# Kernel optimization log

Hardware: AMD Instinct MI355X
Metric: run time of the kernel (lower is better)

Reference implementation:

```python
import jax, jax.numpy as jnp
import numpy as np

THRE = 0.5        # communication threshold
ALPHA = 0.8       # S_e / S_c mix in pattern gate
P_BIAS, P_WEIGHT = 0.1, 0.9
DILATE_K = 3
EPS = 1e-6


def warp_affine(src, M, out_hw):
    """torch F.affine_grid + F.grid_sample (bilinear, zeros padding, align_corners=False).
    src: (B,C,Hs,Ws), M: (B,2,3) normalized affine. Returns (B,C,Ho,Wo)."""
    B, C, Hs, Ws = src.shape
    Ho, Wo = out_hw
    xs = 2.0 * (jnp.arange(Wo, dtype=src.dtype) + 0.5) / Wo - 1.0
    ys = 2.0 * (jnp.arange(Ho, dtype=src.dtype) + 0.5) / Ho - 1.0
    gx, gy = jnp.meshgrid(xs, ys)                                   # (Ho,Wo)
    base = jnp.stack([gx, gy, jnp.ones_like(gx)], axis=-1)          # (Ho,Wo,3)
    g = jnp.einsum('bij,hwj->bhwi', M.astype(src.dtype), base)      # (B,Ho,Wo,2) x,y
    px = ((g[..., 0] + 1.0) * Ws - 1.0) * 0.5
    py = ((g[..., 1] + 1.0) * Hs - 1.0) * 0.5
    x0 = jnp.floor(px); y0 = jnp.floor(py)
    wx1 = px - x0; wx0 = 1.0 - wx1
    wy1 = py - y0; wy0 = 1.0 - wy1
    bidx = jnp.arange(B)[:, None, None]
    def samp(yi, xi):
        yi = yi.astype(jnp.int32); xi = xi.astype(jnp.int32)
        valid = (yi >= 0) & (yi < Hs) & (xi >= 0) & (xi < Ws)
        yc = jnp.clip(yi, 0, Hs - 1); xc = jnp.clip(xi, 0, Ws - 1)
        v = src[bidx, :, yc, xc]                                    # (B,Ho,Wo,C)
        return v * valid[..., None].astype(src.dtype)
    out = (samp(y0, x0) * (wy0 * wx0)[..., None]
         + samp(y0, x0 + 1) * (wy0 * wx1)[..., None]
         + samp(y0 + 1, x0) * (wy1 * wx0)[..., None]
         + samp(y0 + 1, x0 + 1) * (wy1 * wx1)[..., None])
    return jnp.transpose(out, (0, 3, 1, 2))


def masked_quantile(xf, mf, q):
    """torch.quantile(x[mask], q) with linear interpolation. xf:(N,HW) float, mf:(N,HW) bool."""
    xs = jnp.sort(jnp.where(mf, xf, jnp.inf), axis=-1)
    cnt = mf.sum(axis=-1)
    pos = q * jnp.maximum(cnt - 1, 0).astype(xf.dtype)
    lo = jnp.floor(pos).astype(jnp.int32)
    hi = jnp.ceil(pos).astype(jnp.int32)
    frac = pos - lo.astype(xf.dtype)
    vlo = jnp.take_along_axis(xs, lo[:, None], axis=-1)[:, 0]
    vhi = jnp.take_along_axis(xs, hi[:, None], axis=-1)[:, 0]
    val = vlo + frac * (vhi - vlo)
    return jnp.where(cnt > 0, val, jnp.zeros_like(val))


def qnorm01(x, mask, ql=0.2, qh=0.8):
    """_qnorm01_masked: per-image masked quantile normalization to [0,1]."""
    N = x.shape[0]
    xf = x.reshape(N, -1)
    mf = mask.reshape(N, -1) > 0
    lo = masked_quantile(xf, mf, ql)[:, None]
    hi = masked_quantile(xf, mf, qh)[:, None]
    y = jnp.clip((xf - lo) / (hi - lo + EPS), 0.0, 1.0) * mf.astype(x.dtype)
    return y.reshape(x.shape)


def pattern_gate(conf_b, feats_b, vis_b):
    """_build_pattern_gate. Returns P (1,1,H,W) on ego plane."""
    visf = (vis_b > 0).astype(feats_b.dtype)
    energy = jnp.mean(feats_b ** 2, axis=1, keepdims=True)          # (N,1,H,W)
    S_e = qnorm01(energy, vis_b) * visf
    S_c_raw = jnp.max(jax.nn.sigmoid(conf_b), axis=1, keepdims=True)  # A>1 branch
    S_c = qnorm01(S_c_raw, vis_b) * visf
    S_mix = ALPHA * S_e + (1.0 - ALPHA) * S_c
    D_e = qnorm01(1.0 - S_e[0:1], vis_b[0:1])
    D_c = qnorm01(1.0 - S_c[0:1], vis_b[0:1])
    D = (0.7 * D_e + 0.3 * D_c) * visf[0:1]
    m0 = vis_b[0:1].reshape(1, -1) > 0
    q20_e = masked_quantile(S_e[0:1].reshape(1, -1), m0, 0.2)[0]
    q20_c = masked_quantile(S_c[0:1].reshape(1, -1), m0, 0.2)[0]
    Ke = (S_e[0:1] <= q20_e) & (vis_b[0:1] > 0)
    Kc = (S_c[0:1] <= q20_c) & (vis_b[0:1] > 0)
    K_empty = (Ke & Kc).astype(feats_b.dtype)
    Sup_nei = jnp.mean(S_mix[1:] * visf[1:], axis=0, keepdims=True)
    P = D * Sup_nei * (1.0 - K_empty)
    return qnorm01(P, vis_b[0:1]) * visf[0:1]


def dilate(mask, k):
    if k <= 1:
        return mask
    return jax.lax.reduce_window(mask, -jnp.inf, jax.lax.max,
                                 (1, 1, k, k), (1, 1, 1, 1), 'SAME')


def owner_for_batch(feats_b, conf_b, vis_b, base_b):
    """_compute_owner_masks_from_comm for one batch group (N agents), eval mode
    (soft_tau=0 -> hard argmax owner), dual_ratio=0, dilate_k=3, supply='cls'."""
    N = feats_b.shape[0]
    visf = (vis_b > 0).astype(feats_b.dtype)
    S_full = jnp.clip(conf_b, 0.0, 1.0).mean(axis=1, keepdims=True) * visf
    P = pattern_gate(conf_b, feats_b, vis_b)                        # (1,1,H,W)
    S_b = S_full * (P_BIAS + P_WEIGHT * P)                          # broadcast over N
    scores = S_b * visf                                             # (N,1,H,W)
    winner = jnp.argmax(scores, axis=0)                             # (1,H,W)
    onehot = (jnp.arange(N)[:, None, None, None] == winner[None]).astype(feats_b.dtype)
    owner = onehot * (base_b > 0).astype(feats_b.dtype)
    return dilate(owner, DILATE_K)


def forward(x, psm_single, record_len, normalized_affine_matrix):
    B, L = normalized_affine_matrix.shape[:2]
    N = L  # uniform record_len assumed (record_len[b] == L for all b)
    sumN, C, H, W = x.shape
    A = psm_single.shape[1]
    # ego-view warp matrices t_matrix[0, :N] per batch, flattened to (B*N,2,3)
    M = normalized_affine_matrix[:, 0].reshape(B * N, 2, 3)
    ones = jnp.ones((B * N, 1, H, W), x.dtype)
    vis = warp_affine(ones, M, (H, W))          # warp masks
    conf = warp_affine(psm_single, M, (H, W))   # warped confidence maps
    wx = warp_affine(x, M, (H, W))              # warped features
    # Communication: where2comm-style threshold on max-sigmoid confidence; ego always ones
    comm_map = jnp.max(jax.nn.sigmoid(conf), axis=1, keepdims=True)
    comm = (comm_map > THRE).astype(x.dtype)
    comm = comm.reshape(B, N, 1, H, W).at[:, 0].set(1.0)            # (B,N,1,H,W)
    owner = jax.vmap(owner_for_batch)(
        wx.reshape(B, N, C, H, W), conf.reshape(B, N, A, H, W),
        vis.reshape(B, N, 1, H, W), comm)                           # (B,N,1,H,W)
    final = comm * owner
    wxm = wx.reshape(B, N, C, H, W) * final
    # effective rate over non-ego agents
    eff = final[:, 1:].sum(axis=(1, 2, 3, 4)) / ((N - 1) * H * W)
    effective_rate = eff.mean()
    x_out = wxm.max(axis=1)                                         # MaxFusion over agents
    return x_out, effective_rate


def setup_inputs():
    key = jax.random.key(0)
    k1, k2, k3 = jax.random.split(key, 3)
    B, N, C, A, H, W = 4, 5, 64, 2, 128, 256
    x = jax.random.normal(k1, (B * N, C, H, W), jnp.float32)
    psm_single = jax.random.normal(k2, (B * N, A, H, W), jnp.float32)
    record_len = jnp.full((B,), N, jnp.int32)
    eye = jnp.tile(jnp.array([[1.0, 0.0, 0.0], [0.0, 1.0, 0.0]], jnp.float32), (B, N, N, 1, 1))
    mats = eye + 0.05 * jax.random.normal(k3, (B, N, N, 2, 3), jnp.float32)
    return {"x": x, "psm_single": psm_single, "record_len": record_len,
            "normalized_affine_matrix": mats}


def reference(x, psm_single, record_len, normalized_affine_matrix):
    return forward(x, psm_single, record_len, normalized_affine_matrix)
```

## Files before the change

### kernel.cpp

```cpp
#include <hip/hip_runtime.h>

#define W_    256
#define H_    128
#define HW_   32768
#define NB    4
#define NA    5
#define NC    64
#define NIMG  20
#define EPS_  1e-6f

#define TW    32
#define TH    16
#define CAP   2048
#define TRIPS 2
#define NBUF  3

struct Taps { int o00,o01,o10,o11; float w00,w01,w10,w11; };

__device__ inline void proj_pt(float M0,float M1,float M2,float M3,float M4,float M5,
                               int h,int w,float&px,float&py){
  float gx = 2.0f*((float)w+0.5f)/(float)W_ - 1.0f;
  float gy = 2.0f*((float)h+0.5f)/(float)H_ - 1.0f;
  float X = M0*gx + M1*gy + M2;
  float Y = M3*gx + M4*gy + M5;
  px = ((X+1.0f)*(float)W_ - 1.0f)*0.5f;
  py = ((Y+1.0f)*(float)H_ - 1.0f)*0.5f;
}

__device__ inline Taps make_taps(const float* __restrict__ M, int h, int w){
  float px,py; proj_pt(M[0],M[1],M[2],M[3],M[4],M[5],h,w,px,py);
  float x0f=floorf(px), y0f=floorf(py);
  float wx1=px-x0f, wx0=1.f-wx1, wy1=py-y0f, wy0=1.f-wy1;
  int x0=(int)x0f, y0=(int)y0f, x1=x0+1, y1=y0+1;
  bool vx0=(x0>=0)&&(x0<W_), vx1=(x1>=0)&&(x1<W_);
  bool vy0=(y0>=0)&&(y0<H_), vy1=(y1>=0)&&(y1<H_);
  int cx0=min(max(x0,0),W_-1), cx1=min(max(x1,0),W_-1);
  int cy0=min(max(y0,0),H_-1), cy1=min(max(y1,0),H_-1);
  Taps t;
  t.o00=cy0*W_+cx0; t.o01=cy0*W_+cx1; t.o10=cy1*W_+cx0; t.o11=cy1*W_+cx1;
  t.w00=(vy0&&vx0)?(wy0*wx0):0.f;
  t.w01=(vy0&&vx1)?(wy0*wx1):0.f;
  t.w10=(vy1&&vx0)?(wy1*wx0):0.f;
  t.w11=(vy1&&vx1)?(wy1*wx1):0.f;
  return t;
}

__device__ inline float clip01(float v){ return fminf(fmaxf(v,0.f),1.f); }
__device__ inline float sigmoidf_(float v){
  if (v>=0.f){ float e=expf(-v); return 1.f/(1.f+e); }
  float e=expf(v); return e/(1.f+e);
}
__device__ inline float quantv(int cnt, float q, float vlo, float vhi){
  if (cnt<=0) return 0.f;
  float pos = q*(float)(cnt-1);
  float frac = pos - floorf(pos);
  return vlo + frac*(vhi-vlo);
}
__device__ inline float ge_f(float t, float lo, float hi){
  return clip01((t-lo)/(hi-lo+EPS_));
}

#define SBAR __builtin_amdgcn_sched_barrier(0)

__global__ void k_init(int* counters){ if (threadIdx.x < 1+NIMG) counters[threadIdx.x] = 0; }

__global__ __launch_bounds__(256) void k_warp_stats(
  const float* __restrict__ x, const float* __restrict__ psm, const float* __restrict__ nam,
  float* __restrict__ vis, float* __restrict__ scraw, float* __restrict__ sfull,
  float* __restrict__ energy, int* __restrict__ cntv)
{
  __shared__ __align__(16) float smem[NBUF][CAP];
  int tid = threadIdx.x;
  int tx = blockIdx.x, ty = blockIdx.y, bn = blockIdx.z;
  int b = bn/NA, n = bn - b*NA;
  const float* M = nam + (size_t)(b*NA*NA + n)*6;
  float M0=M[0],M1=M[1],M2=M[2],M3=M[3],M4=M[4],M5=M[5];
  int tw0 = tx*TW, th0 = ty*TH;
  int r  = tid>>4;
  int cb = (tid&15)<<1;
  int h  = th0 + r;
  int w0 = tw0 + cb;

  float pxa,pya,pxb,pyb,pxc,pyc,pxd,pyd;
  proj_pt(M0,M1,M2,M3,M4,M5, th0,      tw0,      pxa,pya);
  proj_pt(M0,M1,M2,M3,M4,M5, th0,      tw0+TW-1, pxb,pyb);
  proj_pt(M0,M1,M2,M3,M4,M5, th0+TH-1, tw0,      pxc,pyc);
  proj_pt(M0,M1,M2,M3,M4,M5, th0+TH-1, tw0+TW-1, pxd,pyd);
  float pxmin=fminf(fminf(pxa,pxb),fminf(pxc,pxd));
  float pxmax=fmaxf(fmaxf(pxa,pxb),fmaxf(pxc,pxd));
  float pymin=fminf(fminf(pya,pyb),fminf(pyc,pyd));
  float pymax=fmaxf(fmaxf(pya,pyb),fmaxf(pyc,pyd));
  int xs = min(max((int)floorf(pxmin)-1, 0), W_-1);
  int xe = min(max((int)floorf(pxmax)+2, 0), W_-1);
  int ys = min(max((int)floorf(pymin)-1, 0), H_-1);
  int ye = min(max((int)floorf(pymax)+2, 0), H_-1);
  int xs4 = xs & ~3;
  int bwid = xe - xs4 + 1, bh = ye - ys + 1;
  int nck = (bwid+3)>>2;
  int bwp = nck<<2;
  int E2 = bh*bwp;
  bool ok = (E2 <= CAP);

  float vvv[2], w00_[2],w01_[2],w10_[2],w11_[2];
  int   gx0[2],gx1[2],gy0c[2],gy1c[2];
  int   rx0[2]; bool vx0f[2];
  #pragma unroll
  for (int k=0;k<2;++k){
    float px,py; proj_pt(M0,M1,M2,M3,M4,M5, h, w0+k, px,py);
    float x0f=floorf(px), y0f=floorf(py);
    float wx1=px-x0f, wx0=1.f-wx1, wy1=py-y0f, wy0=1.f-wy1;
    int x0=(int)x0f, y0=(int)y0f, x1=x0+1, y1=y0+1;
    bool vx0=(x0>=0)&&(x0<W_), vx1=(x1>=0)&&(x1<W_);
    bool vy0=(y0>=0)&&(y0<H_), vy1=(y1>=0)&&(y1<H_);
    float w00=(vy0&&vx0)?(wy0*wx0):0.f;
    float w01=(vy0&&vx1)?(wy0*wx1):0.f;
    float w10=(vy1&&vx0)?(wy1*wx0):0.f;
    float w11=(vy1&&vx1)?(wy1*wx1):0.f;
    w00_[k]=w00; w01_[k]=w01; w10_[k]=w10; w11_[k]=w11;
    vvv[k]=w00+w01+w10+w11;
    gx0[k]=min(max(x0,0),W_-1); gx1[k]=min(max(x1,0),W_-1);
    gy0c[k]=min(max(y0,0),H_-1); gy1c[k]=min(max(y1,0),H_-1);
    rx0[k]=x0; vx0f[k]=vx0;
  }

  size_t idx = (size_t)bn*HW_ + (size_t)h*W_ + w0;
  float acc[2] = {0.f,0.f};

  int srcoff[TRIPS]; int ldsbase = (tid>>6)<<6;
  const float* xb0 = x + (size_t)bn*NC*HW_ + (size_t)ys*W_ + xs4;
  if (ok){
    int totq = bh*nck;
    unsigned magic = (unsigned)((0x100000000ULL + (unsigned)nck - 1) / (unsigned)nck);
    int colcap = (W_-4) - xs4;
    #pragma unroll
    for (int k=0;k<TRIPS;++k){
      int qq = min(tid + (k<<8), totq-1);
      int row = (int)__umulhi((unsigned)qq, magic);
      int col = (qq - row*nck)<<2;
      srcoff[k] = row*W_ + min(col, colcap);
    }
  }
  auto issue = [&](int ch, int bsel){
    const float* src = xb0 + (size_t)ch*HW_;
    #pragma unroll
    for (int k=0;k<TRIPS;++k){
      __builtin_amdgcn_global_load_lds(
        (const __attribute__((address_space(1))) void*)(src + srcoff[k]),
        (__attribute__((address_space(3))) void*)&smem[bsel][(ldsbase + (k<<8))<<2],
        16, 0, 0);
    }
  };
  if (ok){ issue(0,0); issue(1,1); }

  {
    const float* p0 = psm + ((size_t)bn*2+0)*HW_;
    const float* p1 = psm + ((size_t)bn*2+1)*HW_;
    int vsum = 0;
    #pragma unroll
    for (int k=0;k<2;++k){
      int o00=gy0c[k]*W_+gx0[k], o01=gy0c[k]*W_+gx1[k];
      int o10=gy1c[k]*W_+gx0[k], o11=gy1c[k]*W_+gx1[k];
      float c0 = w00_[k]*p0[o00]+w01_[k]*p0[o01]+w10_[k]*p0[o10]+w11_[k]*p0[o11];
      float c1 = w00_[k]*p1[o00]+w01_[k]*p1[o01]+w10_[k]*p1[o10]+w11_[k]*p1[o11];
      vis[idx+k]   = vvv[k];
      scraw[idx+k] = fmaxf(sigmoidf_(c0), sigmoidf_(c1));
      sfull[idx+k] = (clip01(c0)+clip01(c1))*0.5f;
      vsum += (vvv[k]>0.f)?1:0;
    }
    #pragma unroll
    for (int off=32;off;off>>=1) vsum += __shfl_down(vsum,off);
    if ((tid&63)==0) atomicAdd(&cntv[bn], vsum);
  }

  if (ok){
    int a0[2],a1[2]; float e0[2],e1[2],f0[2],f1[2];
    #pragma unroll
    for (int k=0;k<2;++k){
      int bc = min(max(rx0[k]-xs4,0), bwp-1);
      a0[k] = (gy0c[k]-ys)*bwp + bc;
      a1[k] = (gy1c[k]-ys)*bwp + bc;
      bool v0 = vx0f[k];
      e0[k] = v0 ? w00_[k] : w01_[k];
      e1[k] = v0 ? w01_[k] : 0.f;
      f0[k] = v0 ? w10_[k] : w11_[k];
      f1[k] = v0 ? w11_[k] : 0.f;
    }
    #pragma unroll 1
    for (int c=0;c<NC;++c){
      asm volatile("s_waitcnt vmcnt(2)" ::: "memory"); SBAR;
      __builtin_amdgcn_s_barrier(); SBAR;
      {
        int nc2 = c+2 < NC ? c+2 : NC-1;
        issue(nc2, (c+2)%NBUF);
      }
      const float* B = smem[c%NBUF];
      #pragma unroll
      for (int k=0;k<2;++k){
        float r00=B[a0[k]], r01=B[a0[k]+1];
        float r10=B[a1[k]], r11=B[a1[k]+1];
        float v = e0[k]*r00 + e1[k]*r01 + f0[k]*r10 + f1[k]*r11;
        acc[k] += v*v;
      }
    }
    asm volatile("s_waitcnt vmcnt(0)" ::: "memory");
  } else {
    const float* xb = x + (size_t)bn*NC*HW_;
    int go00[2],go01[2],go10[2],go11[2];
    #pragma unroll
    for (int k=0;k<2;++k){
      go00[k]=gy0c[k]*W_+gx0[k]; go01[k]=gy0c[k]*W_+gx1[k];
      go10[k]=gy1c[k]*W_+gx0[k]; go11[k]=gy1c[k]*W_+gx1[k];
    }
    for (int c=0;c<NC;++c){
      const float* pc = xb + (size_t)c*HW_;
      #pragma unroll
      for (int k=0;k<2;++k){
        float v = w00_[k]*pc[go00[k]] + w01_[k]*pc[go01[k]]
                + w10_[k]*pc[go10[k]] + w11_[k]*pc[go11[k]];
        acc[k] += v*v;
      }
    }
  }
  #pragma unroll
  for (int k=0;k<2;++k) energy[idx+k] = acc[k]*(1.0f/64.0f);
}

#define OS_T 1024
__global__ __launch_bounds__(1024) void k_select(
    const float* __restrict__ energy, const float* __restrict__ scraw,
    const float* __restrict__ ppre, const float* __restrict__ vis,
    const int* __restrict__ cnts,
    float* __restrict__ statsE, float* __restrict__ statsC, float* __restrict__ statsP,
    int mode)
{
  __shared__ int hist[16*256];
  __shared__ int cum[256];
  __shared__ unsigned s_pre;
  __shared__ int s_rk;
  int tid = threadIdx.x;
  int t = blockIdx.x;

  const float* d; const float* m; float* stats; int img, r, cnt;
  if (mode==0){
    bool isC = (t>=96); int tt = isC ? t-96 : t;
    if (tt<80){ img=tt>>2; r=tt&3; } else { int j=tt-80; img=(j>>2)*NA; r=4+(j&3); }
    d = (isC?scraw:energy) + (size_t)img*HW_;
    m = vis + (size_t)img*HW_;
    stats = isC?statsC:statsE;
    cnt = cnts[img];
  } else {
    img = t>>2; r = t&3;
    d = ppre + (size_t)img*HW_;
    m = vis + (size_t)(img*NA)*HW_;
    stats = statsP;
    cnt = cnts[img*NA];
  }
  int cm1 = cnt>0 ? cnt-1 : 0;
  float p2 = 0.2f*(float)cm1, p8 = 0.8f*(float)cm1;
  int l2=(int)floorf(p2), h2=(int)ceilf(p2), l8=(int)floorf(p8), h8=(int)ceilf(p8);
  int rank;
  switch(r){
    case 0: rank=l2; break;      case 1: rank=h2; break;
    case 2: rank=l8; break;      case 3: rank=h8; break;
    case 4: rank=cm1-l2; break;  case 5: rank=cm1-h2; break;
    case 6: rank=cm1-l8; break;  default: rank=cm1-h8; break;
  }

  unsigned key[32];
  #pragma unroll
  for (int k=0;k<32;++k){
    int i = tid + (k<<10);
    unsigned u = __float_as_uint(d[i]);
    unsigned kk = (u & 0x80000000u) ? ~u : (u|0x80000000u);
    key[k] = (m[i] > 0.f) ? kk : 0xFFFFFFFFu;
  }

  if (tid==0){ s_pre=0u; s_rk=rank; }
  int slice = tid & 15;
  #pragma unroll
  for (int round=0; round<4; ++round){
    const int shift = 24 - 8*round;
    for (int i=tid;i<16*256;i+=OS_T) hist[i]=0;
    __syncthreads();
    unsigned pre = s_pre;
    if (round==0){
      #pragma unroll
      for (int k=0;k<32;++k)
        atomicAdd(&hist[slice*256 + (key[k]>>24)], 1);
    } else {
      #pragma unroll
      for (int k=0;k<32;++k)
        if ((key[k]>>(shift+8)) == pre)
          atomicAdd(&hist[slice*256 + ((key[k]>>shift)&255u)], 1);
    }
    __syncthreads();
    if (tid<256){
      int tt=0;
      #pragma unroll
      for (int s=0;s<16;++s) tt += hist[s*256+tid];
      cum[tid]=tt;
    }
    __syncthreads();
    if (tid<64){
      int c0=cum[4*tid+0],c1=cum[4*tid+1],c2=cum[4*tid+2],c3=cum[4*tid+3];
      int i0=c0, i1=i0+c1, i2=i1+c2, i3=i2+c3;
      int tot=i3, scan=tot;
      #pragma unroll
      for (int off=1;off<64;off<<=1){ int v=__shfl_up(scan,off); if (tid>=off) scan+=v; }
      int base = scan-tot;
      int rk = s_rk; unsigned pr = s_pre;
      int b0=base, b1=base+i0, b2=base+i1, b3=base+i2, e3=base+i3;
      if      (rk>=b0 && rk<b1){ s_pre=(pr<<8)|(unsigned)(4*tid+0); s_rk=rk-b0; }
      else if (rk>=b1 && rk<b2){ s_pre=(pr<<8)|(unsigned)(4*tid+1); s_rk=rk-b1; }
      else if (rk>=b2 && rk<b3){ s_pre=(pr<<8)|(unsigned)(4*tid+2); s_rk=rk-b2; }
      else if (rk>=b3 && rk<e3){ s_pre=(pr<<8)|(unsigned)(4*tid+3); s_rk=rk-b3; }
    }
    __syncthreads();
  }
  if (tid==0){
    unsigned k = s_pre;
    unsigned u = (k & 0x80000000u) ? (k & 0x7FFFFFFFu) : ~k;
    stats[img*16 + 1 + r] = __uint_as_float(u);
    if (r==0) stats[img*16] = (float)cnt;
  }
}

__global__ void k_params(const float* __restrict__ statsE, const float* __restrict__ statsC,
                         float* __restrict__ params){
  int b = threadIdx.x;
  if (b>=NB) return;
  float* pr = params + b*32;
  for (int n=0;n<NA;++n){
    const float* sE = statsE + (size_t)(b*NA+n)*16;
    const float* sC = statsC + (size_t)(b*NA+n)*16;
    int cE=(int)sE[0], cC=(int)sC[0];
    pr[n]    = quantv(cE,0.2f,sE[1],sE[2]);
    pr[5+n]  = quantv(cE,0.8f,sE[3],sE[4]);
    pr[10+n] = quantv(cC,0.2f,sC[1],sC[2]);
    pr[15+n] = quantv(cC,0.8f,sC[3],sC[4]);
  }
  const float* sE0 = statsE + (size_t)(b*NA)*16;
  const float* sC0 = statsC + (size_t)(b*NA)*16;
  float loe=pr[0], hie=pr[5], loc=pr[10], hic=pr[15];
  float de_lo=0.f,de_hi=0.f,ke=0.f, dc_lo=0.f,dc_hi=0.f,kc=0.f;
  int c0=(int)sE0[0];
  if (c0>0){
    int cm1=c0-1;
    float pos2=0.2f*(float)cm1, pos8=0.8f*(float)cm1;
    float f2=pos2-floorf(pos2), f8=pos8-floorf(pos8);
    float a,bb;
    a=1.f-ge_f(sE0[5],loe,hie); bb=1.f-ge_f(sE0[6],loe,hie); de_lo=a+f2*(bb-a);
    a=1.f-ge_f(sE0[7],loe,hie); bb=1.f-ge_f(sE0[8],loe,hie); de_hi=a+f8*(bb-a);
    a=ge_f(sE0[1],loe,hie);     bb=ge_f(sE0[2],loe,hie);     ke  =a+f2*(bb-a);
  }
  int c0c=(int)sC0[0];
  if (c0c>0){
    int cm1=c0c-1;
    float pos2=0.2f*(float)cm1, pos8=0.8f*(float)cm1;
    float f2=pos2-floorf(pos2), f8=pos8-floorf(pos8);
    float a,bb;
    a=1.f-ge_f(sC0[5],loc,hic); bb=1.f-ge_f(sC0[6],loc,hic); dc_lo=a+f2*(bb-a);
    a=1.f-ge_f(sC0[7],loc,hic); bb=1.f-ge_f(sC0[8],loc,hic); dc_hi=a+f8*(bb-a);
    a=ge_f(sC0[1],loc,hic);     bb=ge_f(sC0[2],loc,hic);     kc  =a+f2*(bb-a);
  }
  pr[20]=de_lo; pr[21]=de_hi; pr[22]=dc_lo; pr[23]=dc_hi; pr[24]=ke; pr[25]=kc;
}

__global__ __launch_bounds__(256) void k_ppre(
  const float* __restrict__ vis, const float* __restrict__ scraw,
  const float* __restrict__ energy, const float* __restrict__ params,
  float* __restrict__ ppre)
{
  int w=threadIdx.x, h=blockIdx.x, b=blockIdx.y;
  int p=h*W_+w;
  const float* pr = params + b*32;
  size_t base = (size_t)b*NA*HW_ + p;
  float se[NA], sc[NA], vf[NA];
  #pragma unroll
  for (int n=0;n<NA;++n){
    float vv = vis[base + (size_t)n*HW_];
    float f = (vv>0.f)?1.f:0.f; vf[n]=f;
    se[n] = clip01((energy[base+(size_t)n*HW_]-pr[n])/(pr[5+n]-pr[n]+EPS_))*f;
    sc[n] = clip01((scraw[base+(size_t)n*HW_]-pr[10+n])/(pr[15+n]-pr[10+n]+EPS_))*f;
  }
  float sup = 0.f;
  #pragma unroll
  for (int n=1;n<NA;++n) sup += (0.8f*se[n]+0.2f*sc[n])*vf[n];
  sup *= 0.25f;
  float de = clip01(((1.f-se[0])-pr[20])/(pr[21]-pr[20]+EPS_))*vf[0];
  float dc = clip01(((1.f-sc[0])-pr[22])/(pr[23]-pr[22]+EPS_))*vf[0];
  float D  = (0.7f*de + 0.3f*dc)*vf[0];
  bool ke = (se[0] <= pr[24]) && (vf[0]>0.f);
  bool kc = (sc[0] <= pr[25]) && (vf[0]>0.f);
  float kem = (ke&&kc)?1.f:0.f;
  ppre[(size_t)b*HW_+p] = D*sup*(1.f-kem);
}

__global__ __launch_bounds__(256) void k_owner(
  const float* __restrict__ vis, const float* __restrict__ scraw,
  const float* __restrict__ sfull, const float* __restrict__ ppre,
  const float* __restrict__ statsP, int* __restrict__ omask)
{
  int w=threadIdx.x,h=blockIdx.x,b=blockIdx.y;
  int p=h*W_+w;
  const float* sP = statsP + b*16;
  int cntP=(int)sP[0];
  float plo = quantv(cntP,0.2f,sP[1],sP[2]);
  float phi = quantv(cntP,0.8f,sP[3],sP[4]);
  size_t base=(size_t)b*NA*HW_+p;
  float vf0 = (vis[base]>0.f)?1.f:0.f;
  float Pf = clip01((ppre[(size_t)b*HW_+p]-plo)/(phi-plo+EPS_))*vf0;
  float gate = 0.1f + 0.9f*Pf;
  int winner=0; float best=-1.f;
  int cbits=0;
  #pragma unroll
  for (int n=0;n<NA;++n){
    float vv = vis[base+(size_t)n*HW_];
    float f=(vv>0.f)?1.f:0.f;
    float s = ((sfull[base+(size_t)n*HW_]*f)*gate)*f;
    if (s>best){best=s;winner=n;}
    bool cm = (n==0) || (scraw[base+(size_t)n*HW_] > 0.5f);
    if (cm) cbits |= 1<<n;
  }
  int ob = ((cbits>>winner)&1) ? (1<<winner) : 0;
  omask[(size_t)b*HW_+p] = ob | (cbits<<8);
}

__global__ __launch_bounds__(256) void k_final(
  const int* __restrict__ omask, int* __restrict__ fmask, int* __restrict__ counter)
{
  int w=threadIdx.x,h=blockIdx.x,b=blockIdx.y;
  int p=h*W_+w;
  const int* om = omask + (size_t)b*HW_;
  int ow=0;
  #pragma unroll
  for (int dy=-1;dy<=1;++dy){
    int y=h+dy; if (y<0||y>=H_) continue;
    #pragma unroll
    for (int dx=-1;dx<=1;++dx){
      int x=w+dx; if (x<0||x>=W_) continue;
      ow |= om[y*W_+x];
    }
  }
  int cbits=(om[p]>>8)&31;
  int fin = ow & cbits & 31;
  fmask[(size_t)b*HW_+p]=fin;
  int cn = __popc(fin & 30);
  for (int off=32;off;off>>=1) cn += __shfl_down(cn,off);
  if ((threadIdx.x&63)==0) atomicAdd(counter, cn);
}

__global__ __launch_bounds__(256, 2) void k_out(
  const float* __restrict__ x, const float* __restrict__ nam,
  const int* __restrict__ fmask, const int* __restrict__ counter,
  float* __restrict__ out, int out_size)
{
  int w=threadIdx.x, h=blockIdx.x, b=blockIdx.y;
  int p=h*W_+w;
  int fin = fmask[(size_t)b*HW_+p] & 31;
  float init = (__popc(fin)<NA) ? 0.f : -__builtin_inff();
  Taps tp[NA];
  #pragma unroll
  for (int n=0;n<NA;++n) tp[n] = make_taps(nam + (size_t)(b*NA*NA+n)*6, h, w);
  #pragma unroll 1
  for (int cb=0; cb<NC/16; ++cb){
    float m[16];
    #pragma unroll
    for (int c=0;c<16;++c) m[c]=init;
    #pragma unroll
    for (int n=0;n<NA;++n){
      if (!((fin>>n)&1)) continue;
      const float* pc = x + ((size_t)(b*NA+n)*NC + cb*16)*HW_;
      float a00[16],a01[16],a10[16],a11[16];
      #pragma unroll
      for (int c=0;c<16;++c){
        a00[c]=pc[tp[n].o00]; a01[c]=pc[tp[n].o01]; a10[c]=pc[tp[n].o10]; a11[c]=pc[tp[n].o11];
        pc += HW_;
      }
      #pragma unroll
      for (int c=0;c<16;++c){
        float v = tp[n].w00*a00[c] + tp[n].w01*a01[c] + tp[n].w10*a10[c] + tp[n].w11*a11[c];
        m[c] = fmaxf(m[c], v);
      }
    }
    #pragma unroll
    for (int c=0;c<16;++c)
      out[(((size_t)b*NC + cb*16 + c)*H_+h)*W_+w] = m[c];
  }
  if (b==0 && h==0 && w==0)
    out[out_size-1] = (float)(*counter) * (1.0f/524288.0f);
}

extern "C" void kernel_launch(void* const* d_in, const int* in_sizes, int n_in,
                              void* d_out, int out_size, void* d_ws, size_t ws_size,
                              hipStream_t stream) {
  (void)in_sizes; (void)n_in; (void)ws_size;
  const float* x   = (const float*)d_in[0];
  const float* psm = (const float*)d_in[1];
  const float* nam = (const float*)d_in[3];
  float* out = (float*)d_out;

  float* ws     = (float*)d_ws;
  float* vis    = ws;
  float* scraw  = vis    + (size_t)NIMG*HW_;
  float* sfull  = scraw  + (size_t)NIMG*HW_;
  float* energy = sfull  + (size_t)NIMG*HW_;
  float* ppre   = energy + (size_t)NIMG*HW_;
  float* statsE = ppre   + (size_t)NB*HW_;
  float* statsC = statsE + NIMG*16;
  float* statsP = statsC + NIMG*16;
  float* params = statsP + NB*16;
  int*   omask  = (int*)(params + NB*32);
  int*   fmask  = omask + (size_t)NB*HW_;
  int*   counter= fmask + (size_t)NB*HW_;
  int*   cntv   = counter + 1;

  hipLaunchKernelGGL(k_init, dim3(1), dim3(64), 0, stream, counter);
  hipLaunchKernelGGL(k_warp_stats, dim3(W_/TW, H_/TH, NIMG), dim3(256), 0, stream,
                     x, psm, nam, vis, scraw, sfull, energy, cntv);
  hipLaunchKernelGGL(k_select, dim3(192), dim3(OS_T), 0, stream,
                     energy, scraw, ppre, vis, cntv, statsE, statsC, statsP, 0);
  hipLaunchKernelGGL(k_params, dim3(1), dim3(64), 0, stream, statsE, statsC, params);
  hipLaunchKernelGGL(k_ppre, dim3(H_,NB), dim3(W_), 0, stream,
                     vis, scraw, energy, params, ppre);
  hipLaunchKernelGGL(k_select, dim3(16), dim3(OS_T), 0, stream,
                     energy, scraw, ppre, vis, cntv, statsE, statsC, statsP, 1);
  hipLaunchKernelGGL(k_owner, dim3(H_,NB), dim3(W_), 0, stream,
                     vis, scraw, sfull, ppre, statsP, omask);
  hipLaunchKernelGGL(k_final, dim3(H_,NB), dim3(W_), 0, stream, omask, fmask, counter);
  hipLaunchKernelGGL(k_out, dim3(H_,NB), dim3(W_), 0, stream,
                     x, nam, fmask, counter, out, out_size);
}
```

Measured before the change: 249.6 us.

## Compute warped energy from precomputed local Gram products instead of per-channel sampling

Energy is the channel-mean of the squared bilinear warp. The change expands that square into a quadratic form over the four taps. A new kernel precomputes per-pixel channel sums of squares and of neighbour cross-products (right, down, both diagonals) in a single coalesced pass over x. A second per-pixel kernel then combines these with the bilinear weights, which removes the per-channel LDS-staged gather loop. The cost is five extra full-size workspace buffers and an extra launch, and the fast path only runs when the workspace is large enough; otherwise it falls back to the old kernel.

```diff
diff --git a/kernel.cpp b/kernel.cpp
--- a/kernel.cpp
+++ b/kernel.cpp
@@ -8,12 +8,6 @@
 #define NC    64
 #define NIMG  20
 #define EPS_  1e-6f
-
-#define TW    32
-#define TH    16
-#define CAP   2048
-#define TRIPS 2
-#define NBUF  3
 
 struct Taps { int o00,o01,o10,o11; float w00,w01,w10,w11; };
 
@@ -64,28 +58,124 @@
 
 __global__ void k_init(int* counters){ if (threadIdx.x < 1+NIMG) counters[threadIdx.x] = 0; }
 
-__global__ __launch_bounds__(256) void k_warp_stats(
+__global__ __launch_bounds__(128) void k_gram(
+  const float* __restrict__ x, float* __restrict__ gA, float* __restrict__ gBx,
+  float* __restrict__ gBy, float* __restrict__ gBd1, float* __restrict__ gBd2)
+{
+  int tid = threadIdx.x;
+  int lane = tid & 63;
+  int bx = blockIdx.x;
+  int bn = bx >> 6;
+  int slab = bx & 63;
+  int r  = slab*2 + (tid>>6);
+  int rn = min(r+1, H_-1);
+  int col = lane<<2;
+  const float* xb = x + (size_t)bn*NC*HW_;
+  float4 aA={0,0,0,0}, aBx={0,0,0,0}, aBy={0,0,0,0}, aBd1={0,0,0,0}, aBd2={0,0,0,0};
+  #pragma unroll 4
+  for (int c=0;c<NC;++c){
+    const float* pc = xb + (size_t)c*HW_;
+    float4 a = *reinterpret_cast<const float4*>(pc + r*W_  + col);
+    float4 b = *reinterpret_cast<const float4*>(pc + rn*W_ + col);
+    float axn = __shfl(a.x, lane+1, 64);
+    float bxn = __shfl(b.x, lane+1, 64);
+    aA.x  = fmaf(a.x,a.x,aA.x);  aA.y  = fmaf(a.y,a.y,aA.y);
+    aA.z  = fmaf(a.z,a.z,aA.z);  aA.w  = fmaf(a.w,a.w,aA.w);
+    aBx.x = fmaf(a.x,a.y,aBx.x); aBx.y = fmaf(a.y,a.z,aBx.y);
+    aBx.z = fmaf(a.z,a.w,aBx.z); aBx.w = fmaf(a.w,axn,aBx.w);
+    aBy.x = fmaf(a.x,b.x,aBy.x); aBy.y = fmaf(a.y,b.y,aBy.y);
+    aBy.z = fmaf(a.z,b.z,aBy.z); aBy.w = fmaf(a.w,b.w,aBy.w);
+    aBd1.x= fmaf(a.x,b.y,aBd1.x);aBd1.y= fmaf(a.y,b.z,aBd1.y);
+    aBd1.z= fmaf(a.z,b.w,aBd1.z);aBd1.w= fmaf(a.w,bxn,aBd1.w);
+    aBd2.x= fmaf(a.y,b.x,aBd2.x);aBd2.y= fmaf(a.z,b.y,aBd2.y);
+    aBd2.z= fmaf(a.w,b.z,aBd2.z);aBd2.w= fmaf(axn,b.w,aBd2.w);
+  }
+  size_t o = (size_t)bn*HW_ + (size_t)r*W_ + col;
+  *reinterpret_cast<float4*>(gA +o) = aA;
+  *reinterpret_cast<float4*>(gBx+o) = aBx;
+  *reinterpret_cast<float4*>(gBy+o) = aBy;
+  *reinterpret_cast<float4*>(gBd1+o)= aBd1;
+  *reinterpret_cast<float4*>(gBd2+o)= aBd2;
+}
+
+__global__ __launch_bounds__(256) void k_warp2(
+  const float* __restrict__ psm, const float* __restrict__ nam,
+  const float* __restrict__ gA, const float* __restrict__ gBx,
+  const float* __restrict__ gBy, const float* __restrict__ gBd1,
+  const float* __restrict__ gBd2,
+  float* __restrict__ vis, float* __restrict__ scraw, float* __restrict__ sfull,
+  float* __restrict__ energy, int* __restrict__ cntv)
+{
+  int w = threadIdx.x, h = blockIdx.x, bn = blockIdx.y;
+  int b = bn/NA, n = bn - b*NA;
+  const float* M = nam + (size_t)(b*NA*NA + n)*6;
+  float px,py; proj_pt(M[0],M[1],M[2],M[3],M[4],M[5],h,w,px,py);
+  float x0f=floorf(px), y0f=floorf(py);
+  float wx1=px-x0f, wx0=1.f-wx1, wy1=py-y0f, wy0=1.f-wy1;
+  int x0=(int)x0f, y0=(int)y0f, x1=x0+1, y1=y0+1;
+  bool vx0=(x0>=0)&&(x0<W_), vx1=(x1>=0)&&(x1<W_);
+  bool vy0=(y0>=0)&&(y0<H_), vy1=(y1>=0)&&(y1<H_);
+  int cx0=min(max(x0,0),W_-1), cx1=min(max(x1,0),W_-1);
+  int cy0=min(max(y0,0),H_-1), cy1=min(max(y1,0),H_-1);
+  float w00=(vy0&&vx0)?(wy0*wx0):0.f;
+  float w01=(vy0&&vx1)?(wy0*wx1):0.f;
+  float w10=(vy1&&vx0)?(wy1*wx0):0.f;
+  float w11=(vy1&&vx1)?(wy1*wx1):0.f;
+  int i00=cy0*W_+cx0, i01=cy0*W_+cx1, i10=cy1*W_+cx0, i11=cy1*W_+cx1;
+  float vv = w00+w01+w10+w11;
+
+  const float* p0 = psm + ((size_t)bn*2+0)*HW_;
+  const float* p1 = psm + ((size_t)bn*2+1)*HW_;
+  float c0 = w00*p0[i00]+w01*p0[i01]+w10*p0[i10]+w11*p0[i11];
+  float c1 = w00*p1[i00]+w01*p1[i01]+w10*p1[i10]+w11*p1[i11];
+
+  const float* A  = gA  + (size_t)bn*HW_;
+  const float* Bx = gBx + (size_t)bn*HW_;
+  const float* By = gBy + (size_t)bn*HW_;
+  const float* D1 = gBd1+ (size_t)bn*HW_;
+  const float* D2 = gBd2+ (size_t)bn*HW_;
+  float e = w00*w00*A[i00] + w01*w01*A[i01] + w10*w10*A[i10] + w11*w11*A[i11]
+          + 2.0f*( w00*w01*Bx[i00] + w10*w11*Bx[i10]
+                 + w00*w10*By[i00] + w01*w11*By[i01]
+                 + w00*w11*D1[i00] + w01*w10*D2[i00] );
+
+  size_t idx = (size_t)bn*HW_ + (size_t)h*W_ + w;
+  vis[idx]=vv;
+  scraw[idx]=fmaxf(sigmoidf_(c0), sigmoidf_(c1));
+  sfull[idx]=(clip01(c0)+clip01(c1))*0.5f;
+  energy[idx]=e*(1.0f/64.0f);
+  int vf = (vv>0.f)?1:0;
+  #pragma unroll
+  for (int off=32;off;off>>=1) vf += __shfl_down(vf,off);
+  if ((w&63)==0) atomicAdd(&cntv[bn], vf);
+}
+
+#define TWm    32
+#define THm    16
+#define CAPm   2048
+#define TRIPSm 2
+#define NBUFm  3
+__global__ __launch_bounds__(256) void k_warp_stats_mono(
   const float* __restrict__ x, const float* __restrict__ psm, const float* __restrict__ nam,
   float* __restrict__ vis, float* __restrict__ scraw, float* __restrict__ sfull,
   float* __restrict__ energy, int* __restrict__ cntv)
 {
-  __shared__ __align__(16) float smem[NBUF][CAP];
+  __shared__ __align__(16) float smem[NBUFm][CAPm];
   int tid = threadIdx.x;
   int tx = blockIdx.x, ty = blockIdx.y, bn = blockIdx.z;
   int b = bn/NA, n = bn - b*NA;
   const float* M = nam + (size_t)(b*NA*NA + n)*6;
   float M0=M[0],M1=M[1],M2=M[2],M3=M[3],M4=M[4],M5=M[5];
-  int tw0 = tx*TW, th0 = ty*TH;
+  int tw0 = tx*TWm, th0 = ty*THm;
   int r  = tid>>4;
   int cb = (tid&15)<<1;
   int h  = th0 + r;
   int w0 = tw0 + cb;
-
   float pxa,pya,pxb,pyb,pxc,pyc,pxd,pyd;
-  proj_pt(M0,M1,M2,M3,M4,M5, th0,      tw0,      pxa,pya);
-  proj_pt(M0,M1,M2,M3,M4,M5, th0,      tw0+TW-1, pxb,pyb);
-  proj_pt(M0,M1,M2,M3,M4,M5, th0+TH-1, tw0,      pxc,pyc);
-  proj_pt(M0,M1,M2,M3,M4,M5, th0+TH-1, tw0+TW-1, pxd,pyd);
+  proj_pt(M0,M1,M2,M3,M4,M5, th0,       tw0,       pxa,pya);
+  proj_pt(M0,M1,M2,M3,M4,M5, th0,       tw0+TWm-1, pxb,pyb);
+  proj_pt(M0,M1,M2,M3,M4,M5, th0+THm-1, tw0,       pxc,pyc);
+  proj_pt(M0,M1,M2,M3,M4,M5, th0+THm-1, tw0+TWm-1, pxd,pyd);
   float pxmin=fminf(fminf(pxa,pxb),fminf(pxc,pxd));
   float pxmax=fmaxf(fmaxf(pxa,pxb),fmaxf(pxc,pxd));
   float pymin=fminf(fminf(pya,pyb),fminf(pyc,pyd));
@@ -99,8 +189,7 @@
   int nck = (bwid+3)>>2;
   int bwp = nck<<2;
   int E2 = bh*bwp;
-  bool ok = (E2 <= CAP);
-
+  bool ok = (E2 <= CAPm);
   float vvv[2], w00_[2],w01_[2],w10_[2],w11_[2];
   int   gx0[2],gx1[2],gy0c[2],gy1c[2];
   int   rx0[2]; bool vx0f[2];
@@ -122,18 +211,16 @@
     gy0c[k]=min(max(y0,0),H_-1); gy1c[k]=min(max(y1,0),H_-1);
     rx0[k]=x0; vx0f[k]=vx0;
   }
-
   size_t idx = (size_t)bn*HW_ + (size_t)h*W_ + w0;
   float acc[2] = {0.f,0.f};
-
-  int srcoff[TRIPS]; int ldsbase = (tid>>6)<<6;
+  int srcoff[TRIPSm]; int ldsbase = (tid>>6)<<6;
   const float* xb0 = x + (size_t)bn*NC*HW_ + (size_t)ys*W_ + xs4;
   if (ok){
     int totq = bh*nck;
     unsigned magic = (unsigned)((0x100000000ULL + (unsigned)nck - 1) / (unsigned)nck);
     int colcap = (W_-4) - xs4;
     #pragma unroll
-    for (int k=0;k<TRIPS;++k){
+    for (int k=0;k<TRIPSm;++k){
       int qq = min(tid + (k<<8), totq-1);
       int row = (int)__umulhi((unsigned)qq, magic);
       int col = (qq - row*nck)<<2;
@@ -143,7 +230,7 @@
   auto issue = [&](int ch, int bsel){
     const float* src = xb0 + (size_t)ch*HW_;
     #pragma unroll
-    for (int k=0;k<TRIPS;++k){
+    for (int k=0;k<TRIPSm;++k){
       __builtin_amdgcn_global_load_lds(
         (const __attribute__((address_space(1))) void*)(src + srcoff[k]),
         (__attribute__((address_space(3))) void*)&smem[bsel][(ldsbase + (k<<8))<<2],
@@ -151,7 +238,6 @@
     }
   };
   if (ok){ issue(0,0); issue(1,1); }
-
   {
     const float* p0 = psm + ((size_t)bn*2+0)*HW_;
     const float* p1 = psm + ((size_t)bn*2+1)*HW_;
@@ -171,7 +257,6 @@
     for (int off=32;off;off>>=1) vsum += __shfl_down(vsum,off);
     if ((tid&63)==0) atomicAdd(&cntv[bn], vsum);
   }
-
   if (ok){
     int a0[2],a1[2]; float e0[2],e1[2],f0[2],f1[2];
     #pragma unroll
@@ -191,9 +276,9 @@
       __builtin_amdgcn_s_barrier(); SBAR;
       {
         int nc2 = c+2 < NC ? c+2 : NC-1;
-        issue(nc2, (c+2)%NBUF);
+        issue(nc2, (c+2)%NBUFm);
       }
-      const float* B = smem[c%NBUF];
+      const float* B = smem[c%NBUFm];
       #pragma unroll
       for (int k=0;k<2;++k){
         float r00=B[a0[k]], r01=B[a0[k]+1];
@@ -494,7 +579,7 @@
 extern "C" void kernel_launch(void* const* d_in, const int* in_sizes, int n_in,
                               void* d_out, int out_size, void* d_ws, size_t ws_size,
                               hipStream_t stream) {
-  (void)in_sizes; (void)n_in; (void)ws_size;
+  (void)in_sizes; (void)n_in;
   const float* x   = (const float*)d_in[0];
   const float* psm = (const float*)d_in[1];
   const float* nam = (const float*)d_in[3];
@@ -514,10 +599,24 @@
   int*   fmask  = omask + (size_t)NB*HW_;
   int*   counter= fmask + (size_t)NB*HW_;
   int*   cntv   = counter + 1;
+  float* gA     = (float*)(cntv + 64);
+  float* gBx    = gA  + (size_t)NIMG*HW_;
+  float* gBy    = gBx + (size_t)NIMG*HW_;
+  float* gBd1   = gBy + (size_t)NIMG*HW_;
+  float* gBd2   = gBd1+ (size_t)NIMG*HW_;
+  size_t need = (size_t)((gBd2 + (size_t)NIMG*HW_) - ws) * sizeof(float);
 
   hipLaunchKernelGGL(k_init, dim3(1), dim3(64), 0, stream, counter);
-  hipLaunchKernelGGL(k_warp_stats, dim3(W_/TW, H_/TH, NIMG), dim3(256), 0, stream,
-                     x, psm, nam, vis, scraw, sfull, energy, cntv);
+  if (ws_size >= need){
+    hipLaunchKernelGGL(k_gram, dim3(NIMG*64), dim3(128), 0, stream,
+                       x, gA, gBx, gBy, gBd1, gBd2);
+    hipLaunchKernelGGL(k_warp2, dim3(H_,NIMG), dim3(W_), 0, stream,
+                       psm, nam, gA, gBx, gBy, gBd1, gBd2,
+                       vis, scraw, sfull, energy, cntv);
+  } else {
+    hipLaunchKernelGGL(k_warp_stats_mono, dim3(W_/TWm, H_/THm, NIMG), dim3(256), 0, stream,
+                       x, psm, nam, vis, scraw, sfull, energy, cntv);
+  }
   hipLaunchKernelGGL(k_select, dim3(192), dim3(OS_T), 0, stream,
                      energy, scraw, ppre, vis, cntv, statsE, statsC, statsP, 0);
   hipLaunchKernelGGL(k_params, dim3(1), dim3(64), 0, stream, statsE, statsC, params);
```

After: 296.3 us. 1.19x slower.
